# Optimization experiments

Hardware: AMD Instinct MI355X
Metric: run time of the kernel (lower is better)

## Reference

```python
import jax, jax.numpy as jnp
import numpy as np

N = 50000
E = 250000
NUM_ETYPES = 4
H = 2  # num_heads
EPS = 1e-12


def _gat_conv(x, W, al, ar, b, src, dst):
    # x: (N, in_dim); W: (in_dim, H*D); al/ar/b: (H, D); src/dst: (E,)
    D = al.shape[-1]
    feat = (x @ W).reshape(-1, H, D)            # (N, H, D)
    el = jnp.sum(feat * al, axis=-1)            # (N, H)
    er = jnp.sum(feat * ar, axis=-1)            # (N, H)
    e = jax.nn.leaky_relu(el[src] + er[dst], 0.2)   # (E, H)
    emax = jax.ops.segment_max(e, dst, num_segments=N)
    ex = jnp.exp(e - emax[dst])
    denom = jax.ops.segment_sum(ex, dst, num_segments=N)
    alpha = ex / denom[dst]                     # (E, H) segment softmax over in-edges
    msg = feat[src] * alpha[:, :, None]         # (E, H, D)
    out = jax.ops.segment_sum(msg, dst, num_segments=N)  # (N, H, D)
    return out + b


def _hetero_layer(x, W, al, ar, b, edges):
    # vmap GATConv over the edge-type axis, then HeteroGraphConv aggregate='mean'
    outs = jax.vmap(lambda w, a, r, bb, e: _gat_conv(x, w, a, r, bb, e[0], e[1]))(
        W, al, ar, b, edges)                    # (T, N, H, D)
    return jnp.mean(outs, axis=0)               # (N, H, D)


def _post(v):
    # relu -> F.normalize(dim=1, i.e. across heads) -> dropout(eval: identity) -> mean over heads
    v = jax.nn.relu(v)
    norm = jnp.sqrt(jnp.sum(v * v, axis=1, keepdims=True))
    v = v / jnp.maximum(norm, EPS)
    return jnp.mean(v, axis=1)                  # (N, D)


def setup_inputs() -> dict:
    key = jax.random.key(0)
    ks = jax.random.split(key, 16)
    s = 0.05
    inp = {
        'x': jax.random.normal(ks[0], (N, 23), jnp.float32),
        'edges': jax.random.randint(ks[1], (NUM_ETYPES, 2, E), 0, N, jnp.int32),
        'W0': jax.random.normal(ks[2], (NUM_ETYPES, 23, H * 64), jnp.float32) * s,
        'al0': jax.random.normal(ks[3], (NUM_ETYPES, H, 64), jnp.float32) * s,
        'ar0': jax.random.normal(ks[4], (NUM_ETYPES, H, 64), jnp.float32) * s,
        'b0': jnp.zeros((NUM_ETYPES, H, 64), jnp.float32),
        'W1': jax.random.normal(ks[5], (NUM_ETYPES, 64, H * 64), jnp.float32) * s,
        'al1': jax.random.normal(ks[6], (NUM_ETYPES, H, 64), jnp.float32) * s,
        'ar1': jax.random.normal(ks[7], (NUM_ETYPES, H, 64), jnp.float32) * s,
        'b1': jnp.zeros((NUM_ETYPES, H, 64), jnp.float32),
        'W2': jax.random.normal(ks[8], (NUM_ETYPES, 64, H * 64), jnp.float32) * s,
        'al2': jax.random.normal(ks[9], (NUM_ETYPES, H, 64), jnp.float32) * s,
        'ar2': jax.random.normal(ks[10], (NUM_ETYPES, H, 64), jnp.float32) * s,
        'b2': jnp.zeros((NUM_ETYPES, H, 64), jnp.float32),
    }
    return inp


def reference(x, edges, W0, al0, ar0, b0, W1, al1, ar1, b1, W2, al2, ar2, b2):
    h = x  # feature_by_level, feat_level=0
    h = _post(_hetero_layer(h, W0, al0, ar0, b0, edges))
    h = _post(_hetero_layer(h, W1, al1, ar1, b1, edges))
    h = jnp.mean(_hetero_layer(h, W2, al2, ar2, b2, edges), axis=1)  # (N, out_dim)
    out = jnp.mean(h, axis=0, keepdims=True)    # dgl.mean_nodes, single graph -> (1, out_dim)
    return out
```

## Files before the change

kernel.cpp:

```cpp
#include <hip/hip_runtime.h>

#define NN 50000
#define NE 250000
#define NSCAN_BLKS ((NN + 255)/256)
#define EDGE_BLKS ((4*NE + 255)/256)
#define NBUCK 4
#define BSZ ((NN + NBUCK - 1)/NBUCK)

typedef __attribute__((ext_vector_type(8))) short bf16x8;
typedef __attribute__((ext_vector_type(4))) float f32x4;

__device__ inline ushort f2bf(float f) {
  uint u = __float_as_uint(f);
  return (ushort)((u + 0x7fffu + ((u >> 16) & 1u)) >> 16);
}
__device__ inline float bf2f(ushort b) { return __uint_as_float(((uint)b) << 16); }

__global__ __launch_bounds__(256) void zero_ints(int* __restrict__ p, int n) {
  int i = blockIdx.x*256 + threadIdx.x;
  if (i < n) p[i] = 0;
}
__global__ __launch_bounds__(256) void zero_floats(float* __restrict__ p, int n) {
  int i = blockIdx.x*256 + threadIdx.x;
  if (i < n) p[i] = 0.f;
}

__global__ __launch_bounds__(256) void count_kernel(const int* __restrict__ edges, int* __restrict__ counts) {
  int idx = blockIdx.x*256 + threadIdx.x;
  if (idx >= 4*NE) return;
  int t = idx / NE, e = idx - t*NE;
  int dst = edges[(size_t)t*2*NE + NE + e];
  atomicAdd(&counts[t*NN + dst], 1);
}

__global__ __launch_bounds__(256) void sumdeg_kernel(const int* __restrict__ counts, int* __restrict__ totdeg) {
  int v = blockIdx.x*256 + threadIdx.x;
  if (v < NN) totdeg[v] = counts[v] + counts[NN+v] + counts[2*NN+v] + counts[3*NN+v];
}

__global__ __launch_bounds__(256) void scan1_kernel(const int* __restrict__ in, int* __restrict__ out, int* __restrict__ bsum, int n) {
  __shared__ int sd[256];
  int i = blockIdx.x*256 + threadIdx.x;
  int v = (i < n) ? in[i] : 0;
  sd[threadIdx.x] = v;
  __syncthreads();
  for (int off = 1; off < 256; off <<= 1) {
    int add = (threadIdx.x >= off) ? sd[threadIdx.x - off] : 0;
    __syncthreads();
    sd[threadIdx.x] += add;
    __syncthreads();
  }
  if (i < n) out[i] = sd[threadIdx.x] - v;
  if (threadIdx.x == 255) bsum[blockIdx.x] = sd[255];
}

__global__ __launch_bounds__(1024) void scan2_kernel(int* __restrict__ bsum, int nb) {
  __shared__ int sd[1024];
  int i = threadIdx.x;
  int v = (i < nb) ? bsum[i] : 0;
  sd[i] = v;
  __syncthreads();
  for (int off = 1; off < 1024; off <<= 1) {
    int add = (i >= off) ? sd[i - off] : 0;
    __syncthreads();
    sd[i] += add;
    __syncthreads();
  }
  if (i < nb) bsum[i] = sd[i] - v;
}

__global__ __launch_bounds__(256) void scan3b_kernel(int* __restrict__ rp, const int* __restrict__ bsum, int n, int total) {
  int i = blockIdx.x*256 + threadIdx.x;
  if (i < n) rp[i] += bsum[blockIdx.x];
  if (i == 0) rp[n] = total;
}

__global__ __launch_bounds__(256) void make_cursor_kernel(const int* __restrict__ rp2, const int* __restrict__ counts,
                                                          int* __restrict__ cursor, int4* __restrict__ bnd4) {
  int v = blockIdx.x*256 + threadIdx.x;
  if (v >= NN) return;
  int b = rp2[v];
  int s1 = b  + counts[v];
  int s2 = s1 + counts[NN+v];
  int s3 = s2 + counts[2*NN+v];
  cursor[v] = b; cursor[NN+v] = s1; cursor[2*NN+v] = s2; cursor[3*NN+v] = s3;
  bnd4[v] = make_int4(b, s1, s2, s3);
  if (v == 0) bnd4[NN] = make_int4(4*NE, 4*NE, 4*NE, 4*NE);
}

__global__ __launch_bounds__(256) void scatter_bucketed(const int* __restrict__ edges, int* __restrict__ cursor,
                                                        int* __restrict__ col2) {
  const int b = blockIdx.x / EDGE_BLKS;
  const int idx = (blockIdx.x - b*EDGE_BLKS)*256 + threadIdx.x;
  if (idx >= 4*NE) return;
  const int t = idx / NE, e = idx - t*NE;
  const int dst = edges[(size_t)t*2*NE + NE + e];
  if (dst < b*BSZ || dst >= (b+1)*BSZ) return;
  const int src = edges[(size_t)t*2*NE + e];
  const int pos = atomicAdd(&cursor[t*NN + dst], 1);
  col2[pos] = src;
}

__global__ __launch_bounds__(256) void convert_x_kernel(const float* __restrict__ x, ushort* __restrict__ xpad) {
  int i = blockIdx.x*256 + threadIdx.x;
  if (i >= NN*64) return;
  int k = i & 63, n = i >> 6;
  xpad[i] = (k < 23) ? f2bf(x[n*23 + k]) : (ushort)0;
}

__global__ __launch_bounds__(256) void convert_wb3_kernel(const float* __restrict__ W0, const float* __restrict__ W1,
                                                          const float* __restrict__ W2, ushort* __restrict__ WB3) {
  int i = blockIdx.x*256 + threadIdx.x;
  if (i >= 3*4*128*64) return;
  int l = i / (4*128*64); int r = i - l*(4*128*64);
  int k = r & 63, c = (r >> 6) & 127, t = r >> 13;
  const float* W = (l == 0) ? W0 : (l == 1) ? W1 : W2;
  const int Kin = (l == 0) ? 23 : 64;
  float w = (k < Kin) ? W[((size_t)t*Kin + k)*128 + c] : 0.f;
  WB3[i] = f2bf(w);
}

__global__ __launch_bounds__(256) void walwar3_kernel(const float* __restrict__ W0, const float* __restrict__ W1,
                                                      const float* __restrict__ W2, const float* __restrict__ al0,
                                                      const float* __restrict__ al1, const float* __restrict__ al2,
                                                      const float* __restrict__ ar0, const float* __restrict__ ar1,
                                                      const float* __restrict__ ar2, ushort* __restrict__ wwb3) {
  int i = blockIdx.x*256 + threadIdx.x;
  if (i >= 3*16*64) return;
  int l = i / (16*64); int r = i - l*(16*64);
  int c = r >> 6, k = r & 63;
  int lr = c >> 3, t = (c >> 1) & 3, h = c & 1;
  const float* W  = (l == 0) ? W0 : (l == 1) ? W1 : W2;
  const float* al = (l == 0) ? al0 : (l == 1) ? al1 : al2;
  const float* ar = (l == 0) ? ar0 : (l == 1) ? ar1 : ar2;
  const int Kin = (l == 0) ? 23 : 64;
  float v = 0.f;
  if (k < Kin) {
    const float* A = (lr ? ar : al) + t*128 + h*64;
    const float* wr = W + ((size_t)t*Kin + k)*128 + h*64;
    for (int d = 0; d < 64; ++d) v += wr[d]*A[d];
  }
  wwb3[i] = f2bf(v);
}

__global__ __launch_bounds__(256)
void elk_kernel(const ushort* __restrict__ hbf, const ushort* __restrict__ wwb,
                float* __restrict__ elp, float* __restrict__ erp)
{
  __shared__ ushort BS[16*64];
  __shared__ float sC[16*66];
  const int tid = threadIdx.x;
  if (tid < 128) ((bf16x8*)BS)[tid] = ((const bf16x8*)wwb)[tid];
  __syncthreads();

  const int wv = tid >> 6, lane = tid & 63;
  const int mrow = lane & 15, kq = lane >> 4;
  const int anode = blockIdx.x*64 + wv*16 + mrow;

  const bf16x8 a0 = *(const bf16x8*)(hbf + (size_t)anode*64 + kq*8);
  const bf16x8 a1 = *(const bf16x8*)(hbf + (size_t)anode*64 + 32 + kq*8);
  const bf16x8 b0 = *(const bf16x8*)(BS + mrow*64 + kq*8);
  const bf16x8 b1 = *(const bf16x8*)(BS + mrow*64 + 32 + kq*8);

  f32x4 acc = (f32x4){0.f,0.f,0.f,0.f};
  acc = __builtin_amdgcn_mfma_f32_16x16x32_bf16(a0, b0, acc, 0, 0, 0);
  acc = __builtin_amdgcn_mfma_f32_16x16x32_bf16(a1, b1, acc, 0, 0, 0);

  #pragma unroll
  for (int r = 0; r < 4; ++r) sC[mrow*66 + wv*16 + kq*4 + r] = acc[r];
  __syncthreads();

  const int t = tid >> 6, n = tid & 63;
  const int node = blockIdx.x*64 + n;
  if (node < NN) {
    float2 e2 = make_float2(sC[(t*2+0)*66 + n], sC[(t*2+1)*66 + n]);
    float2 r2 = make_float2(sC[(8+t*2+0)*66 + n], sC[(8+t*2+1)*66 + n]);
    ((float2*)elp)[(size_t)t*NN + node] = e2;
    ((float2*)erp)[(size_t)t*NN + node] = r2;
  }
}

__global__ __launch_bounds__(256)
void gather_kernel(const ushort* __restrict__ hbf, const float* __restrict__ elp,
                   const float* __restrict__ erp, const int* __restrict__ col2,
                   const int4* __restrict__ bnd4, ushort* __restrict__ agg)
{
  const int v = __builtin_amdgcn_readfirstlane(blockIdx.x*4 + (threadIdx.x >> 6));
  const int lane = threadIdx.x & 63;
  const int h2 = lane >> 5;
  const int j  = lane & 31;
  const uint* hb32 = (const uint*)hbf;
  uint* agg32 = (uint*)agg;

  const int4 bb = bnd4[v];
  const int b4 = ((const int*)bnd4)[(v+1)*4];
  const int bounds[5] = {bb.x, bb.y, bb.z, bb.w, b4};

  #pragma unroll
  for (int t = 0; t < 4; ++t) {
    const int lo = bounds[t], hi = bounds[t+1];
    float ox = 0.f, oy = 0.f;
    if (lo < hi) {
      const float2 er2 = ((const float2*)erp)[(size_t)t*NN + v];
      const int cnt2 = (hi - lo - h2 + 1) >> 1;
      float sum0 = 0.f, sum1 = 0.f, tx0 = 0.f, ty0 = 0.f, tx1 = 0.f, ty1 = 0.f;
      for (int k0 = 0; k0 < cnt2; k0 += 4) {
        int s[4];
        #pragma unroll
        for (int u = 0; u < 4; ++u) {
          const int k = k0 + u;
          s[u] = col2[(k < cnt2) ? (lo + h2 + 2*k) : lo];
        }
        float2 e2[4];
        #pragma unroll
        for (int u = 0; u < 4; ++u) e2[u] = ((const float2*)elp)[(size_t)t*NN + s[u]];
        uint w[4];
        #pragma unroll
        for (int u = 0; u < 4; ++u) w[u] = hb32[(uint)s[u]*32u + (uint)j];
        #pragma unroll
        for (int u = 0; u < 4; ++u) {
          float u0 = e2[u].x + er2.x, u1 = e2[u].y + er2.y;
          u0 = (u0 > 0.f) ? u0 : 0.2f*u0;
          u1 = (u1 > 0.f) ? u1 : 0.2f*u1;
          float p0 = __expf(fminf(u0, 80.f));
          float p1 = __expf(fminf(u1, 80.f));
          if (k0 + u >= cnt2) { p0 = 0.f; p1 = 0.f; }
          sum0 += p0; sum1 += p1;
          const float xv0 = __uint_as_float(w[u] << 16);
          const float xv1 = __uint_as_float(w[u] & 0xffff0000u);
          tx0 += p0*xv0; ty0 += p0*xv1;
          tx1 += p1*xv0; ty1 += p1*xv1;
        }
      }
      sum0 += __shfl_xor(sum0, 32); sum1 += __shfl_xor(sum1, 32);
      tx0 += __shfl_xor(tx0, 32);   ty0 += __shfl_xor(ty0, 32);
      tx1 += __shfl_xor(tx1, 32);   ty1 += __shfl_xor(ty1, 32);
      const float i0 = __builtin_amdgcn_rcpf(sum0);
      const float i1 = __builtin_amdgcn_rcpf(sum1);
      ox = h2 ? tx1*i1 : tx0*i0;
      oy = h2 ? ty1*i1 : ty0*i0;
    }
    const uint pk = (uint)f2bf(ox) | ((uint)f2bf(oy) << 16);
    __builtin_nontemporal_store(pk, &agg32[(size_t)(t*NN + v)*64 + h2*32 + j]);
  }
}

__global__ __launch_bounds__(256)
void transform_kernel(const ushort* __restrict__ agg, const ushort* __restrict__ WB,
                      const float* __restrict__ ball, ushort* __restrict__ hout, int post,
                      const ushort* __restrict__ wwbN, float* __restrict__ elp,
                      float* __restrict__ erp, float* __restrict__ accum, int doReduce)
{
  __shared__ ushort WT[2*128*64];
  __shared__ ushort oS[128][72];
  __shared__ float sb[128];
  __shared__ float sred[256];
  const int tid = threadIdx.x;
  if (tid < 128) sb[tid] = 0.25f*(ball[tid] + ball[128+tid] + ball[256+tid] + ball[384+tid]);

  const int wv = tid >> 6, lane = tid & 63;
  const int mrow = lane & 15, kq = lane >> 4;
  const int node0 = blockIdx.x*128;
  const int anode0 = node0 + wv*32 + mrow;

  f32x4 acc[2][8];
  #pragma unroll
  for (int m = 0; m < 2; ++m)
    #pragma unroll
    for (int nb = 0; nb < 8; ++nb) acc[m][nb] = (f32x4){0.f,0.f,0.f,0.f};

  for (int tb = 0; tb < 4; tb += 2) {
    __syncthreads();
    for (int i = tid; i < 2048; i += 256) {
      int row = i >> 3, jj = i & 7;
      bf16x8 val = ((const bf16x8*)WB)[tb*1024 + i];
      *(bf16x8*)((char*)WT + row*128 + ((jj ^ (row & 7))*16)) = val;
    }
    __syncthreads();
    #pragma unroll
    for (int t2 = 0; t2 < 2; ++t2) {
      const int t = tb + t2;
      bf16x8 a[2][4];
      #pragma unroll
      for (int m = 0; m < 2; ++m) {
        const ushort* ar_ = agg + ((size_t)t*NN + anode0 + m*16)*128;
        a[m][0] = __builtin_nontemporal_load((const bf16x8*)(ar_ + kq*8));
        a[m][1] = __builtin_nontemporal_load((const bf16x8*)(ar_ + 32 + kq*8));
        a[m][2] = __builtin_nontemporal_load((const bf16x8*)(ar_ + 64 + kq*8));
        a[m][3] = __builtin_nontemporal_load((const bf16x8*)(ar_ + 96 + kq*8));
      }
      #pragma unroll
      for (int nb = 0; nb < 8; ++nb) {
        const int row = t2*128 + nb*16 + mrow;
        const bf16x8 b0 = *(const bf16x8*)((const char*)WT + row*128 + ((kq       ^ (row&7))*16));
        const bf16x8 b1 = *(const bf16x8*)((const char*)WT + row*128 + (((4 + kq) ^ (row&7))*16));
        const int hs = (nb >> 2)*2;
        #pragma unroll
        for (int m = 0; m < 2; ++m) {
          acc[m][nb] = __builtin_amdgcn_mfma_f32_16x16x32_bf16(a[m][hs],   b0, acc[m][nb], 0, 0, 0);
          acc[m][nb] = __builtin_amdgcn_mfma_f32_16x16x32_bf16(a[m][hs+1], b1, acc[m][nb], 0, 0, 0);
        }
      }
    }
  }

  #pragma unroll
  for (int m = 0; m < 2; ++m) {
    const int nl0 = wv*32 + m*16 + kq*4;
    #pragma unroll
    for (int nb = 0; nb < 4; ++nb) {
      const int d = nb*16 + mrow;
      const float bm0 = sb[d], bm1 = sb[64 + d];
      #pragma unroll
      for (int r = 0; r < 4; ++r) {
        float h0 = 0.25f*acc[m][nb][r]   + bm0;
        float h1 = 0.25f*acc[m][nb+4][r] + bm1;
        float o;
        if (post) {
          h0 = fmaxf(h0, 0.f); h1 = fmaxf(h1, 0.f);
          o = 0.5f*(h0 + h1) / fmaxf(sqrtf(h0*h0 + h1*h1), 1e-12f);
        } else {
          o = 0.5f*(h0 + h1);
        }
        oS[nl0 + r][d] = f2bf(o);
      }
    }
  }
  __syncthreads();

  if (hout) {
    for (int i = tid; i < 128*16; i += 256) {
      const int nl = i >> 4, seg = i & 15;
      const int v = node0 + nl;
      if (v < NN) *(ushort4*)&hout[(size_t)v*64 + seg*4] = *(ushort4*)&oS[nl][seg*4];
    }
  }

  if (wwbN) {
    #pragma unroll
    for (int m2 = 0; m2 < 2; ++m2) {
      const int ng = wv*2 + m2;
      const int arow = ng*16 + mrow;
      const bf16x8 a0 = *(const bf16x8*)&oS[arow][kq*8];
      const bf16x8 a1 = *(const bf16x8*)&oS[arow][32 + kq*8];
      const bf16x8 b0 = *(const bf16x8*)(wwbN + mrow*64 + kq*8);
      const bf16x8 b1 = *(const bf16x8*)(wwbN + mrow*64 + 32 + kq*8);
      f32x4 c = (f32x4){0.f,0.f,0.f,0.f};
      c = __builtin_amdgcn_mfma_f32_16x16x32_bf16(a0, b0, c, 0, 0, 0);
      c = __builtin_amdgcn_mfma_f32_16x16x32_bf16(a1, b1, c, 0, 0, 0);
      const int lr = mrow >> 3, t = (mrow >> 1) & 3, h = mrow & 1;
      float* dst = lr ? erp : elp;
      #pragma unroll
      for (int r = 0; r < 4; ++r) {
        const int v = node0 + ng*16 + kq*4 + r;
        if (v < NN) dst[((size_t)t*NN + v)*2 + h] = c[r];
      }
    }
  }

  if (doReduce) {
    const int d = tid & 63, g = tid >> 6;
    float s = 0.f;
    for (int nl = g; nl < 128; nl += 4)
      if (node0 + nl < NN) s += bf2f(oS[nl][d]);
    sred[tid] = s;
    __syncthreads();
    if (tid < 64)
      atomicAdd(&accum[tid], sred[tid] + sred[tid+64] + sred[tid+128] + sred[tid+192]);
  }
}

__global__ __launch_bounds__(64) void final_out_kernel(const float* __restrict__ accum, float* __restrict__ out) {
  int d = threadIdx.x;
  if (d < 64) out[d] = accum[d] * (1.0f/NN);
}

extern "C" void kernel_launch(void* const* d_in, const int* in_sizes, int n_in,
                              void* d_out, int out_size, void* d_ws, size_t ws_size,
                              hipStream_t stream) {
  const float* x     = (const float*)d_in[0];
  const int*   edges = (const int*)d_in[1];
  const float* W[3]  = {(const float*)d_in[2], (const float*)d_in[6], (const float*)d_in[10]};
  const float* al[3] = {(const float*)d_in[3], (const float*)d_in[7], (const float*)d_in[11]};
  const float* ar[3] = {(const float*)d_in[4], (const float*)d_in[8], (const float*)d_in[12]};
  const float* b[3]  = {(const float*)d_in[5], (const float*)d_in[9], (const float*)d_in[13]};

  char* ws = (char*)d_ws;
  auto up = [](size_t x_) { return (x_ + 255) & ~(size_t)255; };

  const size_t szAgg  = ((size_t)4*NN + 128)*128*sizeof(ushort);
  const size_t szElp  = (size_t)4*NN*2*sizeof(float);
  const size_t szHB   = (size_t)(NN+64)*64*sizeof(ushort);
  const size_t szWB3  = (size_t)3*4*128*64*sizeof(ushort);
  const size_t szWWB3 = (size_t)3*16*64*sizeof(ushort);
  const size_t szCol  = (size_t)4*NE*sizeof(int);
  const size_t szBnd  = (size_t)(NN+1)*sizeof(int4);
  const size_t szI4   = (size_t)4*NN*sizeof(int);
  const size_t szI1   = (size_t)(NN+1)*sizeof(int);

  size_t o = 0;
  ushort* agg    = (ushort*)(ws + o); o += up(szAgg);
  float*  elp    = (float*)(ws + o);  o += up(szElp);
  float*  erp    = (float*)(ws + o);  o += up(szElp);
  ushort* xpad   = (ushort*)(ws + o); o += up(szHB);
  ushort* hbuf   = (ushort*)(ws + o); o += up(szHB);
  ushort* WB3    = (ushort*)(ws + o); o += up(szWB3);
  ushort* wwb3   = (ushort*)(ws + o); o += up(szWWB3);
  float*  accum  = (float*)(ws + o);  o += up(256);
  int*    col2   = (int*)(ws + o);    o += up(szCol);
  int4*   bnd4   = (int4*)(ws + o);   o += up(szBnd);
  int* row_ptr2  = (int*)(ws + o);    o += up(szI1);
  int* totdeg    = (int*)(ws + o);    o += up(szI1);
  int* cursor    = (int*)(ws + o);    o += up(szI4);
  int* counts    = (int*)(ws + o);    o += up(szI4);
  int* bsum      = (int*)(ws + o);    o += up(4096);

  convert_wb3_kernel<<<(3*4*128*64 + 255)/256, 256, 0, stream>>>(W[0], W[1], W[2], WB3);
  walwar3_kernel<<<(3*16*64 + 255)/256, 256, 0, stream>>>(W[0], W[1], W[2], al[0], al[1], al[2],
                                                          ar[0], ar[1], ar[2], wwb3);
  convert_x_kernel<<<(NN*64 + 255)/256, 256, 0, stream>>>(x, xpad);

  zero_ints<<<(4*NN + 255)/256, 256, 0, stream>>>(counts, 4*NN);
  count_kernel<<<EDGE_BLKS, 256, 0, stream>>>(edges, counts);
  sumdeg_kernel<<<NSCAN_BLKS, 256, 0, stream>>>(counts, totdeg);
  scan1_kernel<<<NSCAN_BLKS, 256, 0, stream>>>(totdeg, row_ptr2, bsum, NN);
  scan2_kernel<<<1, 1024, 0, stream>>>(bsum, NSCAN_BLKS);
  scan3b_kernel<<<NSCAN_BLKS, 256, 0, stream>>>(row_ptr2, bsum, NN, 4*NE);
  make_cursor_kernel<<<NSCAN_BLKS, 256, 0, stream>>>(row_ptr2, counts, cursor, bnd4);
  scatter_bucketed<<<NBUCK*EDGE_BLKS, 256, 0, stream>>>(edges, cursor, col2);
  zero_floats<<<1, 64, 0, stream>>>(accum, 64);

  const int gemmGX = (NN + 63)/64;
  const int tfGX   = (NN + 127)/128;

  elk_kernel<<<gemmGX, 256, 0, stream>>>(xpad, wwb3, elp, erp);

  for (int l = 0; l < 3; ++l) {
    const ushort* hin = (l == 0) ? xpad : hbuf;
    const ushort* WB  = WB3 + (size_t)l*4*128*64;
    const ushort* wwbNext = (l < 2) ? (wwb3 + (size_t)(l+1)*16*64) : nullptr;
    gather_kernel<<<NN/4, 256, 0, stream>>>(hin, elp, erp, col2, bnd4, agg);
    transform_kernel<<<tfGX, 256, 0, stream>>>(agg, WB, b[l],
                                               (l < 2) ? hbuf : nullptr, (l < 2) ? 1 : 0,
                                               wwbNext, elp, erp,
                                               accum, (l == 2) ? 1 : 0);
  }

  final_out_kernel<<<1, 64, 0, stream>>>(accum, (float*)d_out);
}
```

Measured before the change: 371.4 us.

## Precompute per-edge attention exponentials in a separate edge-parallel kernel before gather

The CSR edge list now stores (type-offset src, type-offset dst) pairs. A new edge-parallel kernel computes leaky-relu and exp attention weights per edge into a float2 buffer before each layer's gather. The gather then reads the precomputed weights instead of gathering elp and computing exp per edge inline. This takes the random elp gathers and transcendental work out of the latency-bound gather loop. In exchange it adds one kernel launch per layer, an extra 8 MB write and read of edge weights, and doubles the size of the edge index array.

Measured after the change: 369.2 us. No clear change (-0.6%).

```diff
diff --git a/kernel.cpp b/kernel.cpp
--- a/kernel.cpp
+++ b/kernel.cpp
@@ -89,7 +89,7 @@
 }
 
 __global__ __launch_bounds__(256) void scatter_bucketed(const int* __restrict__ edges, int* __restrict__ cursor,
-                                                        int* __restrict__ col2) {
+                                                        int2* __restrict__ cd2) {
   const int b = blockIdx.x / EDGE_BLKS;
   const int idx = (blockIdx.x - b*EDGE_BLKS)*256 + threadIdx.x;
   if (idx >= 4*NE) return;
@@ -98,7 +98,7 @@
   if (dst < b*BSZ || dst >= (b+1)*BSZ) return;
   const int src = edges[(size_t)t*2*NE + e];
   const int pos = atomicAdd(&cursor[t*NN + dst], 1);
-  col2[pos] = src;
+  cd2[pos] = make_int2(t*NN + src, t*NN + dst);
 }
 
 __global__ __launch_bounds__(256) void convert_x_kernel(const float* __restrict__ x, ushort* __restrict__ xpad) {
@@ -181,15 +181,31 @@
 }
 
 __global__ __launch_bounds__(256)
-void gather_kernel(const ushort* __restrict__ hbf, const float* __restrict__ elp,
-                   const float* __restrict__ erp, const int* __restrict__ col2,
-                   const int4* __restrict__ bnd4, ushort* __restrict__ agg)
+void pexp_kernel(const int2* __restrict__ cd2, const float* __restrict__ elp,
+                 const float* __restrict__ erp, float2* __restrict__ pexp2)
+{
+  int q = blockIdx.x*256 + threadIdx.x;
+  if (q >= 4*NE) return;
+  const int2 cd = cd2[q];
+  const float2 e2 = ((const float2*)elp)[cd.x];
+  const float2 r2 = ((const float2*)erp)[cd.y];
+  float u0 = e2.x + r2.x, u1 = e2.y + r2.y;
+  u0 = (u0 > 0.f) ? u0 : 0.2f*u0;
+  u1 = (u1 > 0.f) ? u1 : 0.2f*u1;
+  pexp2[q] = make_float2(__expf(fminf(u0, 80.f)), __expf(fminf(u1, 80.f)));
+}
+
+__global__ __launch_bounds__(256)
+void gather_kernel(const ushort* __restrict__ hbf, const float2* __restrict__ pexp2,
+                   const int2* __restrict__ cd2, const int4* __restrict__ bnd4,
+                   ushort* __restrict__ agg)
 {
   const int v = __builtin_amdgcn_readfirstlane(blockIdx.x*4 + (threadIdx.x >> 6));
   const int lane = threadIdx.x & 63;
   const int h2 = lane >> 5;
   const int j  = lane & 31;
   const uint* hb32 = (const uint*)hbf;
+  const int* cd2x = (const int*)cd2;
   uint* agg32 = (uint*)agg;
 
   const int4 bb = bnd4[v];
@@ -199,31 +215,29 @@
   #pragma unroll
   for (int t = 0; t < 4; ++t) {
     const int lo = bounds[t], hi = bounds[t+1];
+    const int tbase = t*NN;
     float ox = 0.f, oy = 0.f;
     if (lo < hi) {
-      const float2 er2 = ((const float2*)erp)[(size_t)t*NN + v];
       const int cnt2 = (hi - lo - h2 + 1) >> 1;
       float sum0 = 0.f, sum1 = 0.f, tx0 = 0.f, ty0 = 0.f, tx1 = 0.f, ty1 = 0.f;
       for (int k0 = 0; k0 < cnt2; k0 += 4) {
-        int s[4];
+        int qq[4], s[4];
         #pragma unroll
         for (int u = 0; u < 4; ++u) {
           const int k = k0 + u;
-          s[u] = col2[(k < cnt2) ? (lo + h2 + 2*k) : lo];
+          qq[u] = (k < cnt2) ? (lo + h2 + 2*k) : lo;
         }
-        float2 e2[4];
-        #pragma unroll
-        for (int u = 0; u < 4; ++u) e2[u] = ((const float2*)elp)[(size_t)t*NN + s[u]];
+        #pragma unroll
+        for (int u = 0; u < 4; ++u) s[u] = cd2x[(size_t)qq[u]*2];
+        float2 pp[4];
+        #pragma unroll
+        for (int u = 0; u < 4; ++u) pp[u] = pexp2[qq[u]];
         uint w[4];
         #pragma unroll
-        for (int u = 0; u < 4; ++u) w[u] = hb32[(uint)s[u]*32u + (uint)j];
+        for (int u = 0; u < 4; ++u) w[u] = hb32[(uint)(s[u] - tbase)*32u + (uint)j];
         #pragma unroll
         for (int u = 0; u < 4; ++u) {
-          float u0 = e2[u].x + er2.x, u1 = e2[u].y + er2.y;
-          u0 = (u0 > 0.f) ? u0 : 0.2f*u0;
-          u1 = (u1 > 0.f) ? u1 : 0.2f*u1;
-          float p0 = __expf(fminf(u0, 80.f));
-          float p1 = __expf(fminf(u1, 80.f));
+          float p0 = pp[u].x, p1 = pp[u].y;
           if (k0 + u >= cnt2) { p0 = 0.f; p1 = 0.f; }
           sum0 += p0; sum1 += p1;
           const float xv0 = __uint_as_float(w[u] << 16);
@@ -241,7 +255,7 @@
       oy = h2 ? ty1*i1 : ty0*i0;
     }
     const uint pk = (uint)f2bf(ox) | ((uint)f2bf(oy) << 16);
-    __builtin_nontemporal_store(pk, &agg32[(size_t)(t*NN + v)*64 + h2*32 + j]);
+    __builtin_nontemporal_store(pk, &agg32[(size_t)(tbase + v)*64 + h2*32 + j]);
   }
 }
 
@@ -393,7 +407,8 @@
   const size_t szHB   = (size_t)(NN+64)*64*sizeof(ushort);
   const size_t szWB3  = (size_t)3*4*128*64*sizeof(ushort);
   const size_t szWWB3 = (size_t)3*16*64*sizeof(ushort);
-  const size_t szCol  = (size_t)4*NE*sizeof(int);
+  const size_t szCd2  = (size_t)4*NE*sizeof(int2);
+  const size_t szPex  = (size_t)4*NE*sizeof(float2);
   const size_t szBnd  = (size_t)(NN+1)*sizeof(int4);
   const size_t szI4   = (size_t)4*NN*sizeof(int);
   const size_t szI1   = (size_t)(NN+1)*sizeof(int);
@@ -407,7 +422,8 @@
   ushort* WB3    = (ushort*)(ws + o); o += up(szWB3);
   ushort* wwb3   = (ushort*)(ws + o); o += up(szWWB3);
   float*  accum  = (float*)(ws + o);  o += up(256);
-  int*    col2   = (int*)(ws + o);    o += up(szCol);
+  int2*   cd2    = (int2*)(ws + o);   o += up(szCd2);
+  float2* pexp2  = (float2*)(ws + o); o += up(szPex);
   int4*   bnd4   = (int4*)(ws + o);   o += up(szBnd);
   int* row_ptr2  = (int*)(ws + o);    o += up(szI1);
   int* totdeg    = (int*)(ws + o);    o += up(szI1);
@@ -427,7 +443,7 @@
   scan2_kernel<<<1, 1024, 0, stream>>>(bsum, NSCAN_BLKS);
   scan3b_kernel<<<NSCAN_BLKS, 256, 0, stream>>>(row_ptr2, bsum, NN, 4*NE);
   make_cursor_kernel<<<NSCAN_BLKS, 256, 0, stream>>>(row_ptr2, counts, cursor, bnd4);
-  scatter_bucketed<<<NBUCK*EDGE_BLKS, 256, 0, stream>>>(edges, cursor, col2);
+  scatter_bucketed<<<NBUCK*EDGE_BLKS, 256, 0, stream>>>(edges, cursor, cd2);
   zero_floats<<<1, 64, 0, stream>>>(accum, 64);
 
   const int gemmGX = (NN + 63)/64;
@@ -439,7 +455,8 @@
     const ushort* hin = (l == 0) ? xpad : hbuf;
     const ushort* WB  = WB3 + (size_t)l*4*128*64;
     const ushort* wwbNext = (l < 2) ? (wwb3 + (size_t)(l+1)*16*64) : nullptr;
-    gather_kernel<<<NN/4, 256, 0, stream>>>(hin, elp, erp, col2, bnd4, agg);
+    pexp_kernel<<<EDGE_BLKS, 256, 0, stream>>>(cd2, elp, erp, pexp2);
+    gather_kernel<<<NN/4, 256, 0, stream>>>(hin, pexp2, cd2, bnd4, agg);
     transform_kernel<<<tfGX, 256, 0, stream>>>(agg, WB, b[l],
                                                (l < 2) ? hbuf : nullptr, (l < 2) ? 1 : 0,
                                                wwbNext, elp, erp,
```
